# Kernel tuning notes

Hardware: AMD Instinct MI355X
Metric: run time of the kernel (lower is better)

The kernel has to match this reference:

```python
import jax, jax.numpy as jnp
import numpy as np

N, C, HW = 32, 256, 64          # batch, in_channels, input_size
K = 128                          # n_clusters
S = 8                            # blocks per side
BLOCK = (HW + S - 1) // S        # = 8, padding_size = 0


def setup_inputs() -> dict:
    key = jax.random.key(0)
    k1, k2 = jax.random.split(key)
    x = jax.random.normal(k1, (N, C, HW, HW), dtype=jnp.float32)
    cluster_centers = jax.random.normal(k2, (K, C), dtype=jnp.float32)
    return {"x": x, "cluster_centers": cluster_centers}


def reference(x, cluster_centers):
    # --- Codebook: argmin over squared distances, computed without the
    x2 = jnp.sum(x * x, axis=1)                       # (N, H, W)
    c2 = jnp.sum(cluster_centers * cluster_centers, axis=1)  # (K,)
    xc = jnp.einsum('nchw,kc->nkhw', x, cluster_centers)     # (N, K, H, W)
    dist = x2[:, None] - 2.0 * xc + c2[None, :, None, None]
    code = jnp.argmin(dist, axis=1)                   # (N, H, W) int

    # --- BlockWiseHistogramEncoder: unfold into S*S non-overlapping
    # BLOCKxBLOCK blocks (padding_size == 0 here), one_hot(code+1), mean ---
    shifted = code + 1                                # values in [1, K]
    n = shifted.shape[0]
    blocks = shifted.reshape(n, S, BLOCK, S, BLOCK)
    blocks = blocks.transpose(0, 1, 3, 2, 4).reshape(n, S * S, BLOCK * BLOCK)
    onehot = (blocks[..., None] == jnp.arange(K + 1)).astype(jnp.float32)
    return onehot.mean(axis=2)                        # (N, S*S, K+1)
```

## Files before the change

### kernel.cpp

```cpp
#include <hip/hip_runtime.h>

#define C_DIM 256
#define K_DIM 128
#define HW_DIM 64
#define PIX 4096
#define N_IMG 32
#define ROWU 40

using short8 = __attribute__((ext_vector_type(8))) short;
using f32x4  = __attribute__((ext_vector_type(4))) float;

__device__ __forceinline__ unsigned rne_bf16(float v) {
    unsigned u = __float_as_uint(v);
    return (u + 0x7fffu + ((u >> 16) & 1u)) >> 16;
}
__device__ __forceinline__ float bf_up(unsigned h) { return __uint_as_float(h << 16); }

__device__ __forceinline__ void split3(float v, unsigned& h, unsigned& m, unsigned& l) {
    h = rne_bf16(v);
    float r1 = v - bf_up(h);
    m = rne_bf16(r1);
    float r2 = r1 - bf_up(m);
    l = rne_bf16(r2);
}

__device__ __forceinline__ unsigned long long umin64(unsigned long long a, unsigned long long b) {
    return a < b ? a : b;
}
__device__ __forceinline__ unsigned mono(float d) {
    unsigned u = __float_as_uint(d);
    return u ^ ((u & 0x80000000u) ? 0xFFFFFFFFu : 0x80000000u);
}

__global__ __launch_bounds__(64) void prep_kernel(const float* __restrict__ cl,
                                                  unsigned short* __restrict__ Bt,
                                                  float* __restrict__ c2) {
    int k = blockIdx.x;
    int lane = threadIdx.x;
    const float4* row = (const float4*)(cl + k * C_DIM);
    float4 v = row[lane];
    float vv[4] = {v.x, v.y, v.z, v.w};
    unsigned short* bk = Bt + k * 768 + lane * 4;
#pragma unroll
    for (int i = 0; i < 4; ++i) {
        unsigned h, m, l;
        split3(vv[i], h, m, l);
        bk[i]       = (unsigned short)h;
        bk[256 + i] = (unsigned short)m;
        bk[512 + i] = (unsigned short)l;
    }
    if (lane == 0) {
        float s = 0.f;
#pragma unroll
        for (int i = 0; i < C_DIM / 4; ++i) {
            float4 u = row[i];
            s = fmaf(u.x, u.x, s);
            s = fmaf(u.y, u.y, s);
            s = fmaf(u.z, u.z, s);
            s = fmaf(u.w, u.w, s);
        }
        c2[k] = s;
    }
}

__global__ __launch_bounds__(256) void main_kernel(
    const float* __restrict__ x, const unsigned short* __restrict__ Bt,
    const float* __restrict__ c2v, unsigned char* __restrict__ code) {

    __shared__ __align__(16) unsigned short Ap[3][128 * ROWU];
    __shared__ float x2p[2][128];
    __shared__ unsigned long long red[4][128];

    const int t    = threadIdx.x;
    const int lane = t & 63;
    const int w    = t >> 6;
    const int q    = lane >> 4;
    const int l15  = lane & 15;

    const int px = t & 127;
    const int h  = t >> 7;

    const int b   = blockIdx.x;
    const int img = b >> 5;
    const int pb  = (b & 31) * 128;

    const float* xg = x + (size_t)img * (C_DIM * PIX) + pb + px;

    f32x4 acc[8][2];
#pragma unroll
    for (int m = 0; m < 8; ++m)
#pragma unroll
        for (int ns = 0; ns < 2; ++ns) acc[m][ns] = (f32x4){0.f, 0.f, 0.f, 0.f};

    float xr[16];
#pragma unroll
    for (int j = 0; j < 16; ++j) xr[j] = xg[(size_t)(h * 16 + j) * PIX];

    float x2part = 0.f;
    const unsigned short* btb = Bt + (w * 32 + l15) * 768 + q * 8;

    short8 bv[3][2];

#pragma unroll 1
    for (int ci = 0; ci < 8; ++ci) {
#pragma unroll
        for (int p = 0; p < 3; ++p) {
            bv[p][0] = *(const short8*)(btb + p * 256 + ci * 32);
            bv[p][1] = *(const short8*)(btb + 16 * 768 + p * 256 + ci * 32);
        }

#pragma unroll
        for (int g = 0; g < 2; ++g) {
            unsigned pk0[4], pk1[4], pk2[4];
#pragma unroll
            for (int jj = 0; jj < 4; ++jj) {
                float v0 = xr[g * 8 + jj * 2], v1 = xr[g * 8 + jj * 2 + 1];
                unsigned h0, m0, l0, h1, m1, l1;
                split3(v0, h0, m0, l0);
                split3(v1, h1, m1, l1);
                pk0[jj] = h0 | (h1 << 16);
                pk1[jj] = m0 | (m1 << 16);
                pk2[jj] = l0 | (l1 << 16);
                x2part = fmaf(v0, v0, x2part);
                x2part = fmaf(v1, v1, x2part);
            }
            int base = px * ROWU + h * 16 + g * 8;
            *(uint4*)&Ap[0][base] = make_uint4(pk0[0], pk0[1], pk0[2], pk0[3]);
            *(uint4*)&Ap[1][base] = make_uint4(pk1[0], pk1[1], pk1[2], pk1[3]);
            *(uint4*)&Ap[2][base] = make_uint4(pk2[0], pk2[1], pk2[2], pk2[3]);
        }
        if (ci == 7) x2p[h][px] = x2part;

        if (ci < 7) {
#pragma unroll
            for (int j = 0; j < 16; ++j)
                xr[j] = xg[(size_t)((ci + 1) * 32 + h * 16 + j) * PIX];
        }

        __syncthreads();

#pragma unroll
        for (int pa = 0; pa < 3; ++pa) {
            const int npb = (pa == 0) ? 3 : ((pa == 1) ? 2 : 1);
#pragma unroll
            for (int m = 0; m < 8; ++m) {
                short8 af = *(const short8*)&Ap[pa][(m * 16 + l15) * ROWU + q * 8];
#pragma unroll
                for (int pb2 = 0; pb2 < 3; ++pb2) {
                    if (pb2 < npb) {
                        acc[m][0] = __builtin_amdgcn_mfma_f32_16x16x32_bf16(af, bv[pb2][0], acc[m][0], 0, 0, 0);
                        acc[m][1] = __builtin_amdgcn_mfma_f32_16x16x32_bf16(af, bv[pb2][1], acc[m][1], 0, 0, 0);
                    }
                }
            }
        }
        __syncthreads();
    }

    const float c2a0 = c2v[w * 32 + l15];
    const float c2a1 = c2v[w * 32 + 16 + l15];
    const unsigned n0 = (unsigned)(w * 32 + l15);
    const unsigned n1 = n0 + 16;

#pragma unroll
    for (int m = 0; m < 8; ++m) {
#pragma unroll
        for (int r = 0; r < 4; ++r) {
            int pxl = m * 16 + q * 4 + r;
            float x2v = x2p[0][pxl] + x2p[1][pxl];
            float d0 = (x2v - 2.0f * acc[m][0][r]) + c2a0;
            float d1 = (x2v - 2.0f * acc[m][1][r]) + c2a1;
            unsigned long long k0 = ((unsigned long long)mono(d0) << 32) | n0;
            unsigned long long k1 = ((unsigned long long)mono(d1) << 32) | n1;
            unsigned long long best = umin64(k0, k1);
            best = umin64(best, __shfl_xor(best, 1));
            best = umin64(best, __shfl_xor(best, 2));
            best = umin64(best, __shfl_xor(best, 4));
            best = umin64(best, __shfl_xor(best, 8));
            if (l15 == 0) red[w][pxl] = best;
        }
    }
    __syncthreads();

    if (t < 128) {
        unsigned long long m0 = umin64(umin64(red[0][t], red[1][t]),
                                       umin64(red[2][t], red[3][t]));
        code[(size_t)img * PIX + pb + t] = (unsigned char)(m0 & 0xFFu);
    }
}

__global__ __launch_bounds__(256) void hist_kernel(const unsigned char* __restrict__ code,
                                                   float* __restrict__ out) {
    __shared__ int hist[4][K_DIM + 1];
    int wid = threadIdx.x >> 6, lane = threadIdx.x & 63;
    int b = blockIdx.x * 4 + wid;
    int n = b >> 6, sy = (b >> 3) & 7, sx = b & 7;

    hist[wid][lane] = 0;
    hist[wid][lane + 64] = 0;
    if (lane == 0) hist[wid][128] = 0;
    __syncthreads();

    int hh = sy * 8 + (lane >> 3);
    int ww = sx * 8 + (lane & 7);
    int c = code[n * PIX + hh * HW_DIM + ww];
    atomicAdd(&hist[wid][c + 1], 1);
    __syncthreads();

    const float inv = 1.0f / 64.0f;
    out[(size_t)b * (K_DIM + 1) + lane] = hist[wid][lane] * inv;
    out[(size_t)b * (K_DIM + 1) + 64 + lane] = hist[wid][lane + 64] * inv;
    if (lane == 0) out[(size_t)b * (K_DIM + 1) + 128] = hist[wid][128] * inv;
}

extern "C" void kernel_launch(void* const* d_in, const int* in_sizes, int n_in,
                              void* d_out, int out_size, void* d_ws, size_t ws_size,
                              hipStream_t stream) {
    const float* x  = (const float*)d_in[0];
    const float* cl = (const float*)d_in[1];
    float* out = (float*)d_out;

    unsigned short* Bt = (unsigned short*)d_ws;
    float* c2 = (float*)((char*)d_ws + 196608);
    unsigned char* code = (unsigned char*)d_ws + 197120;

    prep_kernel<<<K_DIM, 64, 0, stream>>>(cl, Bt, c2);
    main_kernel<<<(N_IMG * PIX) / 128, 256, 0, stream>>>(x, Bt, c2, code);
    hist_kernel<<<(N_IMG * 64) / 4, 256, 0, stream>>>(code, out);
}
```

Measured before the change: 228.2 us.

## Store A fragments in MFMA lane order, truncate-split bf16, reuse LDS for reduction

The LDS A tile moves from a padded row-major layout to a fragment-ordered layout, so each lane's 16-byte MFMA operand read is contiguous and conflict-free. The three-way bf16 split now uses truncation instead of round-to-nearest-even, which cuts ALU work per element at a small cost in split accuracy. The argmin reduction buffer now aliases the A tile, shrinking LDS use. `__syncthreads` is replaced by an inline `s_waitcnt lgkmcnt(0)` plus `s_barrier`, and MFMAs are interleaved over pairs of m tiles.

```diff
diff --git a/kernel.cpp b/kernel.cpp
--- a/kernel.cpp
+++ b/kernel.cpp
@@ -5,23 +5,12 @@
 #define HW_DIM 64
 #define PIX 4096
 #define N_IMG 32
-#define ROWU 40
 
 using short8 = __attribute__((ext_vector_type(8))) short;
 using f32x4  = __attribute__((ext_vector_type(4))) float;
 
-__device__ __forceinline__ unsigned rne_bf16(float v) {
-    unsigned u = __float_as_uint(v);
-    return (u + 0x7fffu + ((u >> 16) & 1u)) >> 16;
-}
-__device__ __forceinline__ float bf_up(unsigned h) { return __uint_as_float(h << 16); }
-
-__device__ __forceinline__ void split3(float v, unsigned& h, unsigned& m, unsigned& l) {
-    h = rne_bf16(v);
-    float r1 = v - bf_up(h);
-    m = rne_bf16(r1);
-    float r2 = r1 - bf_up(m);
-    l = rne_bf16(r2);
+__device__ __forceinline__ void lds_barrier() {
+    asm volatile("s_waitcnt lgkmcnt(0)\n\ts_barrier" ::: "memory");
 }
 
 __device__ __forceinline__ unsigned long long umin64(unsigned long long a, unsigned long long b) {
@@ -30,6 +19,16 @@
 __device__ __forceinline__ unsigned mono(float d) {
     unsigned u = __float_as_uint(d);
     return u ^ ((u & 0x80000000u) ? 0xFFFFFFFFu : 0x80000000u);
+}
+
+__device__ __forceinline__ void split3t(float v, unsigned& hu, unsigned& mu, unsigned& lu) {
+    unsigned u = __float_as_uint(v);
+    unsigned hf = u & 0xffff0000u;
+    float r1 = v - __uint_as_float(hf);
+    unsigned r1u = __float_as_uint(r1);
+    unsigned mf = r1u & 0xffff0000u;
+    float r2 = r1 - __uint_as_float(mf);
+    hu = u; mu = r1u; lu = __float_as_uint(r2);
 }
 
 __global__ __launch_bounds__(64) void prep_kernel(const float* __restrict__ cl,
@@ -43,11 +42,11 @@
     unsigned short* bk = Bt + k * 768 + lane * 4;
 #pragma unroll
     for (int i = 0; i < 4; ++i) {
-        unsigned h, m, l;
-        split3(vv[i], h, m, l);
-        bk[i]       = (unsigned short)h;
-        bk[256 + i] = (unsigned short)m;
-        bk[512 + i] = (unsigned short)l;
+        unsigned hu, mu, lu;
+        split3t(vv[i], hu, mu, lu);
+        bk[i]       = (unsigned short)(hu >> 16);
+        bk[256 + i] = (unsigned short)(mu >> 16);
+        bk[512 + i] = (unsigned short)(lu >> 16);
     }
     if (lane == 0) {
         float s = 0.f;
@@ -67,9 +66,9 @@
     const float* __restrict__ x, const unsigned short* __restrict__ Bt,
     const float* __restrict__ c2v, unsigned char* __restrict__ code) {
 
-    __shared__ __align__(16) unsigned short Ap[3][128 * ROWU];
+    __shared__ __align__(16) unsigned short Ap[3 * 4096];
     __shared__ float x2p[2][128];
-    __shared__ unsigned long long red[4][128];
+    unsigned long long* red = (unsigned long long*)Ap;
 
     const int t    = threadIdx.x;
     const int lane = t & 63;
@@ -99,10 +98,11 @@
     float x2part = 0.f;
     const unsigned short* btb = Bt + (w * 32 + l15) * 768 + q * 8;
 
-    short8 bv[3][2];
+    const int wbase = (px >> 4) * 512 + (px & 15) * 8 + h * 2 * 128;
 
 #pragma unroll 1
     for (int ci = 0; ci < 8; ++ci) {
+        short8 bv[3][2];
 #pragma unroll
         for (int p = 0; p < 3; ++p) {
             bv[p][0] = *(const short8*)(btb + p * 256 + ci * 32);
@@ -111,23 +111,23 @@
 
 #pragma unroll
         for (int g = 0; g < 2; ++g) {
-            unsigned pk0[4], pk1[4], pk2[4];
+            unsigned p0[4], p1[4], p2[4];
 #pragma unroll
             for (int jj = 0; jj < 4; ++jj) {
                 float v0 = xr[g * 8 + jj * 2], v1 = xr[g * 8 + jj * 2 + 1];
                 unsigned h0, m0, l0, h1, m1, l1;
-                split3(v0, h0, m0, l0);
-                split3(v1, h1, m1, l1);
-                pk0[jj] = h0 | (h1 << 16);
-                pk1[jj] = m0 | (m1 << 16);
-                pk2[jj] = l0 | (l1 << 16);
+                split3t(v0, h0, m0, l0);
+                split3t(v1, h1, m1, l1);
+                p0[jj] = (h0 >> 16) | (h1 & 0xffff0000u);
+                p1[jj] = (m0 >> 16) | (m1 & 0xffff0000u);
+                p2[jj] = (l0 >> 16) | (l1 & 0xffff0000u);
                 x2part = fmaf(v0, v0, x2part);
                 x2part = fmaf(v1, v1, x2part);
             }
-            int base = px * ROWU + h * 16 + g * 8;
-            *(uint4*)&Ap[0][base] = make_uint4(pk0[0], pk0[1], pk0[2], pk0[3]);
-            *(uint4*)&Ap[1][base] = make_uint4(pk1[0], pk1[1], pk1[2], pk1[3]);
-            *(uint4*)&Ap[2][base] = make_uint4(pk2[0], pk2[1], pk2[2], pk2[3]);
+            int base = wbase + g * 128;
+            *(uint4*)&Ap[base]            = make_uint4(p0[0], p0[1], p0[2], p0[3]);
+            *(uint4*)&Ap[4096 + base]     = make_uint4(p1[0], p1[1], p1[2], p1[3]);
+            *(uint4*)&Ap[8192 + base]     = make_uint4(p2[0], p2[1], p2[2], p2[3]);
         }
         if (ci == 7) x2p[h][px] = x2part;
 
@@ -137,24 +137,27 @@
                 xr[j] = xg[(size_t)((ci + 1) * 32 + h * 16 + j) * PIX];
         }
 
-        __syncthreads();
+        lds_barrier();
 
 #pragma unroll
         for (int pa = 0; pa < 3; ++pa) {
-            const int npb = (pa == 0) ? 3 : ((pa == 1) ? 2 : 1);
-#pragma unroll
-            for (int m = 0; m < 8; ++m) {
-                short8 af = *(const short8*)&Ap[pa][(m * 16 + l15) * ROWU + q * 8];
+#pragma unroll
+            for (int mg = 0; mg < 4; ++mg) {
+                const int m0 = mg * 2, m1 = mg * 2 + 1;
+                short8 af0 = *(const short8*)&Ap[pa * 4096 + m0 * 512 + lane * 8];
+                short8 af1 = *(const short8*)&Ap[pa * 4096 + m1 * 512 + lane * 8];
 #pragma unroll
                 for (int pb2 = 0; pb2 < 3; ++pb2) {
-                    if (pb2 < npb) {
-                        acc[m][0] = __builtin_amdgcn_mfma_f32_16x16x32_bf16(af, bv[pb2][0], acc[m][0], 0, 0, 0);
-                        acc[m][1] = __builtin_amdgcn_mfma_f32_16x16x32_bf16(af, bv[pb2][1], acc[m][1], 0, 0, 0);
+                    if (pb2 < 3 - pa) {
+                        acc[m0][0] = __builtin_amdgcn_mfma_f32_16x16x32_bf16(af0, bv[pb2][0], acc[m0][0], 0, 0, 0);
+                        acc[m0][1] = __builtin_amdgcn_mfma_f32_16x16x32_bf16(af0, bv[pb2][1], acc[m0][1], 0, 0, 0);
+                        acc[m1][0] = __builtin_amdgcn_mfma_f32_16x16x32_bf16(af1, bv[pb2][0], acc[m1][0], 0, 0, 0);
+                        acc[m1][1] = __builtin_amdgcn_mfma_f32_16x16x32_bf16(af1, bv[pb2][1], acc[m1][1], 0, 0, 0);
                     }
                 }
             }
         }
-        __syncthreads();
+        lds_barrier();
     }
 
     const float c2a0 = c2v[w * 32 + l15];
@@ -177,14 +180,14 @@
             best = umin64(best, __shfl_xor(best, 2));
             best = umin64(best, __shfl_xor(best, 4));
             best = umin64(best, __shfl_xor(best, 8));
-            if (l15 == 0) red[w][pxl] = best;
-        }
-    }
-    __syncthreads();
+            if (l15 == 0) red[w * 128 + pxl] = best;
+        }
+    }
+    lds_barrier();
 
     if (t < 128) {
-        unsigned long long m0 = umin64(umin64(red[0][t], red[1][t]),
-                                       umin64(red[2][t], red[3][t]));
+        unsigned long long m0 = umin64(umin64(red[t], red[128 + t]),
+                                       umin64(red[256 + t], red[384 + t]));
         code[(size_t)img * PIX + pb + t] = (unsigned char)(m0 & 0xFFu);
     }
 }
```

New measurement: 226.3 us. About the same (-0.8%).
